# Kernel tuning notes

Measured on AMD Instinct MI355X. Metric: run time of the kernel, lower is better.

Reference implementation:

```python
import jax, jax.numpy as jnp
import numpy as np

GROUP_SIZE = 128


def _dequant_weight(qweight, scales, qzeros, group_size=GROUP_SIZE):
    # qweight: [K//2, N] int, packed nibbles; scales: [K//g, N] fp16; qzeros: [K//2g, N] int
    low = (qweight & 15).astype(jnp.float16)
    high = ((qweight >> 4) & 15).astype(jnp.float16)
    K2, N = qweight.shape
    # interleave even rows = low nibble, odd rows = high nibble -> [K, N]
    w_q = jnp.stack([low, high], axis=1).reshape(2 * K2, N)
    zlow = (qzeros & 15).astype(jnp.float16)
    zhigh = ((qzeros >> 4) & 15).astype(jnp.float16)
    G2, _ = qzeros.shape
    zeros = jnp.stack([zlow, zhigh], axis=1).reshape(2 * G2, N)  # [K//g, N]
    scales_exp = jnp.repeat(scales, group_size, axis=0)          # [K, N]
    zeros_exp = jnp.repeat(zeros, group_size, axis=0)            # [K, N]
    return (w_q - zeros_exp) * scales_exp


def setup_inputs() -> dict:
    key = jax.random.key(0)
    k1, k2, k3, k4 = jax.random.split(key, 4)
    B, S, K, N = 4, 2048, 4096, 11008
    x = jax.random.normal(k1, (B, S, K), dtype=jnp.float16)
    qweight = jax.random.randint(k2, (K // 2, N), 0, 127, dtype=jnp.int32)
    scales = jax.random.uniform(k3, (K // GROUP_SIZE, N), dtype=jnp.float16, minval=0.001, maxval=0.02)
    qzeros = jax.random.randint(k4, (K // GROUP_SIZE // 2, N), 0, 127, dtype=jnp.int32)
    return {"x": x, "qweight": qweight, "scales": scales, "qzeros": qzeros}


def reference(x, qweight, scales, qzeros):
    W = _dequant_weight(qweight, scales, qzeros)  # [K, N] fp16
    return jnp.matmul(x, W)  # [B, S, N]
```

## Files before the change

### kernel.cpp

```cpp
#include <hip/hip_runtime.h>
#include <cstdint>
#include <cstddef>
#include <type_traits>


typedef __bf16 bf16x8 __attribute__((ext_vector_type(8)));
typedef _Float16 halfx8 __attribute__((ext_vector_type(8)));
typedef float floatx4 __attribute__((ext_vector_type(4)));
struct u4 { unsigned x, y, z, w; };

#define M_DIM 8192
#define K_DIM 4096
#define N_DIM 11008
#define BM 128
#define BN 128
#define BK 32

__device__ __forceinline__ unsigned short f2bf(float f) {
  unsigned u = __float_as_uint(f);
  return (unsigned short)((u + 0x7FFFu + ((u >> 16) & 1u)) >> 16);
}
__device__ __forceinline__ float bf2f(unsigned s) { return __uint_as_float(s << 16); }
__device__ __forceinline__ unsigned short f2h(float f) {
  _Float16 h = (_Float16)f;
  return __builtin_bit_cast(unsigned short, h);
}
__device__ __forceinline__ float h2f(unsigned short s) {
  return (float)__builtin_bit_cast(_Float16, s);
}

__global__ void dtype_probe(const unsigned* __restrict__ sd, int* __restrict__ flag) {
  const unsigned lo = sd[threadIdx.x] & 0xFFFFu;
  const int is_bf = (lo >= 0x3A00u) && (lo < 0x3D00u);
  const int is_h  = (lo >= 0x1400u) && (lo < 0x2600u);
  const int f = __all(is_bf) ? 0 : (__all(is_h) ? 2 : 1);
  flag[0] = f;
}

template <int DT>
__launch_bounds__(256, 3)
__global__ void int4gemm_kernel(const void* __restrict__ xv,
                                const int* __restrict__ qw,
                                const void* __restrict__ sv,
                                const int* __restrict__ qz,
                                void* __restrict__ outv,
                                const int* __restrict__ flag) {
  if (*flag != DT) return;

  __shared__ unsigned short As[BM][BK];
  __shared__ unsigned Bs[BN][BK / 2 + 4];
  __shared__ float zoff[32][BN];
  __shared__ float scl[32][BN];

  const int t = threadIdx.x;
  const int m0 = blockIdx.x * BM;
  const int n0 = blockIdx.y * BN;

  for (int i = t; i < 32 * BN; i += 256) {
    const int g = i >> 7, j = i & (BN - 1);
    const int n = n0 + j;
    float s;
    if constexpr (DT == 0)
      s = bf2f(((const unsigned short*)sv)[(size_t)g * N_DIM + n]);
    else if constexpr (DT == 1)
      s = ((const float*)sv)[(size_t)g * N_DIM + n];
    else
      s = h2f(((const unsigned short*)sv)[(size_t)g * N_DIM + n]);
    const int zp = qz[(size_t)(g >> 1) * N_DIM + n];
    const int z = (zp >> ((g & 1) * 4)) & 15;
    zoff[g][j] = 8388608.0f + (float)z;
    scl[g][j] = s;
  }

  const int lane = t & 63;
  const int wid = t >> 6;
  const int wm = (wid >> 1) * 64, wn = (wid & 1) * 64;
  const int lrow = lane & 15, lq = lane >> 4;

  const int mcol = t & 31;
  const int rrow = t >> 5;

  const int c0 = t, c1 = t + 256;

  floatx4 acc[4][4];
#pragma unroll
  for (int mi = 0; mi < 4; ++mi)
#pragma unroll
    for (int ni = 0; ni < 4; ++ni) {
      acc[mi][ni][0] = 0.0f; acc[mi][ni][1] = 0.0f;
      acc[mi][ni][2] = 0.0f; acc[mi][ni][3] = 0.0f;
    }

  __syncthreads();

#pragma unroll 1
  for (int kt = 0; kt < K_DIM / BK; ++kt) {
    const int k0 = kt * BK;

    if constexpr (DT == 1) {
      const float* b0 = (const float*)xv + (size_t)(m0 + (c0 >> 2)) * K_DIM + k0 + ((c0 & 3) << 3);
      const float* b1 = (const float*)xv + (size_t)(m0 + (c1 >> 2)) * K_DIM + k0 + ((c1 & 3) << 3);
      float f0[8], f1[8];
#pragma unroll
      for (int q = 0; q < 8; ++q) f0[q] = b0[q];
#pragma unroll
      for (int q = 0; q < 8; ++q) f1[q] = b1[q];
      u4 p0v, p1v;
      p0v.x = (unsigned)f2bf(f0[0]) | ((unsigned)f2bf(f0[1]) << 16);
      p0v.y = (unsigned)f2bf(f0[2]) | ((unsigned)f2bf(f0[3]) << 16);
      p0v.z = (unsigned)f2bf(f0[4]) | ((unsigned)f2bf(f0[5]) << 16);
      p0v.w = (unsigned)f2bf(f0[6]) | ((unsigned)f2bf(f0[7]) << 16);
      p1v.x = (unsigned)f2bf(f1[0]) | ((unsigned)f2bf(f1[1]) << 16);
      p1v.y = (unsigned)f2bf(f1[2]) | ((unsigned)f2bf(f1[3]) << 16);
      p1v.z = (unsigned)f2bf(f1[4]) | ((unsigned)f2bf(f1[5]) << 16);
      p1v.w = (unsigned)f2bf(f1[6]) | ((unsigned)f2bf(f1[7]) << 16);
      *reinterpret_cast<u4*>(&As[c0 >> 2][(c0 & 3) << 3]) = p0v;
      *reinterpret_cast<u4*>(&As[c1 >> 2][(c1 & 3) << 3]) = p1v;
    } else {
      const unsigned short* xb = (const unsigned short*)xv;
      const u4 a0 = *reinterpret_cast<const u4*>(
          xb + (size_t)(m0 + (c0 >> 2)) * K_DIM + k0 + ((c0 & 3) << 3));
      const u4 a1 = *reinterpret_cast<const u4*>(
          xb + (size_t)(m0 + (c1 >> 2)) * K_DIM + k0 + ((c1 & 3) << 3));
      *reinterpret_cast<u4*>(&As[c0 >> 2][(c0 & 3) << 3]) = a0;
      *reinterpret_cast<u4*>(&As[c1 >> 2][(c1 & 3) << 3]) = a1;
    }

    const int g = k0 >> 7;
    const int* q0 = qw + (size_t)((k0 >> 1) + rrow) * N_DIM + n0 + mcol;
    const int* q1 = q0 + (size_t)8 * N_DIM;
    int p0[4], p1[4];
#pragma unroll
    for (int j = 0; j < 4; ++j) p0[j] = q0[32 * j];
#pragma unroll
    for (int j = 0; j < 4; ++j) p1[j] = q1[32 * j];

#pragma unroll
    for (int j = 0; j < 4; ++j) {
      const int n = mcol + 32 * j;
      const float zo = zoff[g][n], s = scl[g][n];
      const float fl0 = (__uint_as_float((unsigned)(p0[j] & 15) | 0x4B000000u) - zo) * s;
      const float fh0 = (__uint_as_float((unsigned)((p0[j] >> 4) & 15) | 0x4B000000u) - zo) * s;
      const float fl1 = (__uint_as_float((unsigned)(p1[j] & 15) | 0x4B000000u) - zo) * s;
      const float fh1 = (__uint_as_float((unsigned)((p1[j] >> 4) & 15) | 0x4B000000u) - zo) * s;
      unsigned lo0, hi0, lo1, hi1;
      if constexpr (DT == 2) {
        lo0 = f2h(fl0); hi0 = f2h(fh0); lo1 = f2h(fl1); hi1 = f2h(fh1);
      } else {
        lo0 = f2bf(fl0); hi0 = f2bf(fh0); lo1 = f2bf(fl1); hi1 = f2bf(fh1);
      }
      Bs[n][rrow] = lo0 | (hi0 << 16);
      Bs[n][rrow + 8] = lo1 | (hi1 << 16);
    }
    __syncthreads();

    using vecT = typename std::conditional<DT == 2, halfx8, bf16x8>::type;
    vecT av[4], bv[4];
#pragma unroll
    for (int mi = 0; mi < 4; ++mi)
      av[mi] = *reinterpret_cast<const vecT*>(&As[wm + mi * 16 + lrow][lq * 8]);
#pragma unroll
    for (int ni = 0; ni < 4; ++ni)
      bv[ni] = *reinterpret_cast<const vecT*>(&Bs[wn + ni * 16 + lrow][lq * 4]);
#pragma unroll
    for (int mi = 0; mi < 4; ++mi)
#pragma unroll
      for (int ni = 0; ni < 4; ++ni) {
        if constexpr (DT == 2)
          acc[mi][ni] = __builtin_amdgcn_mfma_f32_16x16x32_f16(av[mi], bv[ni],
                                                               acc[mi][ni], 0, 0, 0);
        else
          acc[mi][ni] = __builtin_amdgcn_mfma_f32_16x16x32_bf16(av[mi], bv[ni],
                                                                acc[mi][ni], 0, 0, 0);
      }
    __syncthreads();
  }

#pragma unroll
  for (int mi = 0; mi < 4; ++mi) {
#pragma unroll
    for (int rr = 0; rr < 4; ++rr) {
      const size_t rowoff = (size_t)(m0 + wm + mi * 16 + lq * 4 + rr) * N_DIM;
#pragma unroll
      for (int ni = 0; ni < 4; ++ni) {
        const size_t idx = rowoff + n0 + wn + ni * 16 + lrow;
        const float v = acc[mi][ni][rr];
        if constexpr (DT == 0)
          ((unsigned short*)outv)[idx] = f2bf(v);
        else if constexpr (DT == 1)
          ((float*)outv)[idx] = v;
        else
          ((unsigned short*)outv)[idx] = f2h(v);
      }
    }
  }
}

extern "C" void kernel_launch(void* const* d_in, const int* in_sizes, int n_in,
                              void* d_out, int out_size, void* d_ws, size_t ws_size,
                              hipStream_t stream) {
  const void* x = d_in[0];
  const int* qw = (const int*)d_in[1];
  const void* sc = d_in[2];
  const int* qz = (const int*)d_in[3];
  int* flag = (int*)d_ws;

  dtype_probe<<<1, 64, 0, stream>>>((const unsigned*)sc, flag);

  dim3 grid(M_DIM / BM, N_DIM / BN);
  int4gemm_kernel<0><<<grid, dim3(256), 0, stream>>>(x, qw, sc, qz, d_out, flag);
  int4gemm_kernel<1><<<grid, dim3(256), 0, stream>>>(x, qw, sc, qz, d_out, flag);
  int4gemm_kernel<2><<<grid, dim3(256), 0, stream>>>(x, qw, sc, qz, d_out, flag);
}
```

Before: 1.808 ms.

## Load A tile via global_load_lds with swizzle, packed fp16 dequant, occupancy 4

Activations are now copied straight from global memory into LDS with global_load_lds, using an XOR swizzle on the column slot to avoid bank conflicts. The read side uses the matching swizzled offset. The fp16 path dequantizes two nibbles at once with packed half math, using the 0x6400 magic-number trick and a combined scale/zero table, and the bf16 paths use the hardware v_cvt_pk_bf16_f32 instruction. Launch bounds are raised to 4 waves per SIMD and the shared-memory tables are shrunk so that occupancy can fit. The tradeoffs are tighter register pressure and fp16 rounding in the dequant subtraction.

Result: faster. 1.738 ms (-3.8%).

```diff
diff --git a/kernel.cpp b/kernel.cpp
--- a/kernel.cpp
+++ b/kernel.cpp
@@ -6,6 +6,7 @@
 
 typedef __bf16 bf16x8 __attribute__((ext_vector_type(8)));
 typedef _Float16 halfx8 __attribute__((ext_vector_type(8)));
+typedef _Float16 h2 __attribute__((ext_vector_type(2)));
 typedef float floatx4 __attribute__((ext_vector_type(4)));
 struct u4 { unsigned x, y, z, w; };
 
@@ -28,6 +29,11 @@
 __device__ __forceinline__ float h2f(unsigned short s) {
   return (float)__builtin_bit_cast(_Float16, s);
 }
+__device__ __forceinline__ unsigned cvt_pk_bf16(float lo, float hi) {
+  unsigned r;
+  asm("v_cvt_pk_bf16_f32 %0, %1, %2" : "=v"(r) : "v"(lo), "v"(hi));
+  return r;
+}
 
 __global__ void dtype_probe(const unsigned* __restrict__ sd, int* __restrict__ flag) {
   const unsigned lo = sd[threadIdx.x] & 0xFFFFu;
@@ -38,7 +44,7 @@
 }
 
 template <int DT>
-__launch_bounds__(256, 3)
+__launch_bounds__(256, 4)
 __global__ void int4gemm_kernel(const void* __restrict__ xv,
                                 const int* __restrict__ qw,
                                 const void* __restrict__ sv,
@@ -47,10 +53,9 @@
                                 const int* __restrict__ flag) {
   if (*flag != DT) return;
 
-  __shared__ unsigned short As[BM][BK];
-  __shared__ unsigned Bs[BN][BK / 2 + 4];
-  __shared__ float zoff[32][BN];
-  __shared__ float scl[32][BN];
+  __shared__ __align__(16) unsigned short As[BM * BK];
+  __shared__ __align__(16) unsigned Bs[BN][BK / 2 + 4];
+  __shared__ unsigned tbl[(DT == 2) ? (32 * BN) : (64 * BN)];
 
   const int t = threadIdx.x;
   const int m0 = blockIdx.x * BM;
@@ -59,28 +64,38 @@
   for (int i = t; i < 32 * BN; i += 256) {
     const int g = i >> 7, j = i & (BN - 1);
     const int n = n0 + j;
-    float s;
-    if constexpr (DT == 0)
-      s = bf2f(((const unsigned short*)sv)[(size_t)g * N_DIM + n]);
-    else if constexpr (DT == 1)
-      s = ((const float*)sv)[(size_t)g * N_DIM + n];
-    else
-      s = h2f(((const unsigned short*)sv)[(size_t)g * N_DIM + n]);
     const int zp = qz[(size_t)(g >> 1) * N_DIM + n];
     const int z = (zp >> ((g & 1) * 4)) & 15;
-    zoff[g][j] = 8388608.0f + (float)z;
-    scl[g][j] = s;
+    if constexpr (DT == 2) {
+      const unsigned sb = ((const unsigned short*)sv)[(size_t)g * N_DIM + n];
+      tbl[i] = sb | ((unsigned)f2h(1024.0f + (float)z) << 16);
+    } else {
+      float s;
+      if constexpr (DT == 0)
+        s = bf2f(((const unsigned short*)sv)[(size_t)g * N_DIM + n]);
+      else
+        s = ((const float*)sv)[(size_t)g * N_DIM + n];
+      tbl[i] = __float_as_uint(8388608.0f + (float)z);
+      tbl[32 * BN + i] = __float_as_uint(s);
+    }
   }
 
   const int lane = t & 63;
   const int wid = t >> 6;
   const int wm = (wid >> 1) * 64, wn = (wid & 1) * 64;
   const int lrow = lane & 15, lq = lane >> 4;
+  const int aslot = ((lq ^ ((lrow >> 1) & 3)) << 3);
 
   const int mcol = t & 31;
   const int rrow = t >> 5;
 
-  const int c0 = t, c1 = t + 256;
+  const int arow = t >> 2;
+  const int acol = (((t & 3) ^ ((arow >> 1) & 3)) << 3);
+  const unsigned short* xb = (const unsigned short*)xv;
+  const unsigned short* ga0 = xb + (size_t)(m0 + arow) * K_DIM + acol;
+  const unsigned short* ga1 = ga0 + (size_t)64 * K_DIM;
+  char* lA0 = (char*)As + (wid << 10);
+  char* lA1 = lA0 + 4096;
 
   floatx4 acc[4][4];
 #pragma unroll
@@ -96,35 +111,6 @@
 #pragma unroll 1
   for (int kt = 0; kt < K_DIM / BK; ++kt) {
     const int k0 = kt * BK;
-
-    if constexpr (DT == 1) {
-      const float* b0 = (const float*)xv + (size_t)(m0 + (c0 >> 2)) * K_DIM + k0 + ((c0 & 3) << 3);
-      const float* b1 = (const float*)xv + (size_t)(m0 + (c1 >> 2)) * K_DIM + k0 + ((c1 & 3) << 3);
-      float f0[8], f1[8];
-#pragma unroll
-      for (int q = 0; q < 8; ++q) f0[q] = b0[q];
-#pragma unroll
-      for (int q = 0; q < 8; ++q) f1[q] = b1[q];
-      u4 p0v, p1v;
-      p0v.x = (unsigned)f2bf(f0[0]) | ((unsigned)f2bf(f0[1]) << 16);
-      p0v.y = (unsigned)f2bf(f0[2]) | ((unsigned)f2bf(f0[3]) << 16);
-      p0v.z = (unsigned)f2bf(f0[4]) | ((unsigned)f2bf(f0[5]) << 16);
-      p0v.w = (unsigned)f2bf(f0[6]) | ((unsigned)f2bf(f0[7]) << 16);
-      p1v.x = (unsigned)f2bf(f1[0]) | ((unsigned)f2bf(f1[1]) << 16);
-      p1v.y = (unsigned)f2bf(f1[2]) | ((unsigned)f2bf(f1[3]) << 16);
-      p1v.z = (unsigned)f2bf(f1[4]) | ((unsigned)f2bf(f1[5]) << 16);
-      p1v.w = (unsigned)f2bf(f1[6]) | ((unsigned)f2bf(f1[7]) << 16);
-      *reinterpret_cast<u4*>(&As[c0 >> 2][(c0 & 3) << 3]) = p0v;
-      *reinterpret_cast<u4*>(&As[c1 >> 2][(c1 & 3) << 3]) = p1v;
-    } else {
-      const unsigned short* xb = (const unsigned short*)xv;
-      const u4 a0 = *reinterpret_cast<const u4*>(
-          xb + (size_t)(m0 + (c0 >> 2)) * K_DIM + k0 + ((c0 & 3) << 3));
-      const u4 a1 = *reinterpret_cast<const u4*>(
-          xb + (size_t)(m0 + (c1 >> 2)) * K_DIM + k0 + ((c1 & 3) << 3));
-      *reinterpret_cast<u4*>(&As[c0 >> 2][(c0 & 3) << 3]) = a0;
-      *reinterpret_cast<u4*>(&As[c1 >> 2][(c1 & 3) << 3]) = a1;
-    }
 
     const int g = k0 >> 7;
     const int* q0 = qw + (size_t)((k0 >> 1) + rrow) * N_DIM + n0 + mcol;
@@ -135,22 +121,55 @@
 #pragma unroll
     for (int j = 0; j < 4; ++j) p1[j] = q1[32 * j];
 
+    if constexpr (DT != 1) {
+      __builtin_amdgcn_global_load_lds(
+          (const __attribute__((address_space(1))) unsigned*)(ga0 + k0),
+          (__attribute__((address_space(3))) unsigned*)lA0, 16, 0, 0);
+      __builtin_amdgcn_global_load_lds(
+          (const __attribute__((address_space(1))) unsigned*)(ga1 + k0),
+          (__attribute__((address_space(3))) unsigned*)lA1, 16, 0, 0);
+    } else {
+      const float* xf = (const float*)xv;
+      const float* gf0 = xf + (size_t)(m0 + arow) * K_DIM + k0 + acol;
+      const float* gf1 = gf0 + (size_t)64 * K_DIM;
+      floatx4 fa = *(const floatx4*)gf0, fb = *(const floatx4*)(gf0 + 4);
+      floatx4 fc = *(const floatx4*)gf1, fd = *(const floatx4*)(gf1 + 4);
+      u4 p0v, p1v;
+      p0v.x = cvt_pk_bf16(fa[0], fa[1]); p0v.y = cvt_pk_bf16(fa[2], fa[3]);
+      p0v.z = cvt_pk_bf16(fb[0], fb[1]); p0v.w = cvt_pk_bf16(fb[2], fb[3]);
+      p1v.x = cvt_pk_bf16(fc[0], fc[1]); p1v.y = cvt_pk_bf16(fc[2], fc[3]);
+      p1v.z = cvt_pk_bf16(fd[0], fd[1]); p1v.w = cvt_pk_bf16(fd[2], fd[3]);
+      *reinterpret_cast<u4*>((char*)As + t * 16) = p0v;
+      *reinterpret_cast<u4*>((char*)As + t * 16 + 4096) = p1v;
+    }
+
 #pragma unroll
     for (int j = 0; j < 4; ++j) {
       const int n = mcol + 32 * j;
-      const float zo = zoff[g][n], s = scl[g][n];
-      const float fl0 = (__uint_as_float((unsigned)(p0[j] & 15) | 0x4B000000u) - zo) * s;
-      const float fh0 = (__uint_as_float((unsigned)((p0[j] >> 4) & 15) | 0x4B000000u) - zo) * s;
-      const float fl1 = (__uint_as_float((unsigned)(p1[j] & 15) | 0x4B000000u) - zo) * s;
-      const float fh1 = (__uint_as_float((unsigned)((p1[j] >> 4) & 15) | 0x4B000000u) - zo) * s;
-      unsigned lo0, hi0, lo1, hi1;
       if constexpr (DT == 2) {
-        lo0 = f2h(fl0); hi0 = f2h(fh0); lo1 = f2h(fl1); hi1 = f2h(fh1);
+        const unsigned ts = tbl[(g << 7) + n];
+        const unsigned s2 = __builtin_amdgcn_perm(ts, ts, 0x01000100u);
+        const unsigned z2 = __builtin_amdgcn_perm(ts, ts, 0x03020302u);
+        const h2 zh = __builtin_bit_cast(h2, z2);
+        const h2 sh = __builtin_bit_cast(h2, s2);
+        const unsigned P0 = (unsigned)p0[j], P1 = (unsigned)p1[j];
+        const unsigned q20 = ((P0 & 15u) | ((P0 << 12) & 0xF0000u)) | 0x64006400u;
+        const unsigned q21 = ((P1 & 15u) | ((P1 << 12) & 0xF0000u)) | 0x64006400u;
+        const h2 w0 = (__builtin_bit_cast(h2, q20) - zh) * sh;
+        const h2 w1 = (__builtin_bit_cast(h2, q21) - zh) * sh;
+        Bs[n][rrow] = __builtin_bit_cast(unsigned, w0);
+        Bs[n][rrow + 8] = __builtin_bit_cast(unsigned, w1);
       } else {
-        lo0 = f2bf(fl0); hi0 = f2bf(fh0); lo1 = f2bf(fl1); hi1 = f2bf(fh1);
+        const float zo = __uint_as_float(tbl[(g << 7) + n]);
+        const float s = __uint_as_float(tbl[32 * BN + (g << 7) + n]);
+        const unsigned P0 = (unsigned)p0[j], P1 = (unsigned)p1[j];
+        const float fl0 = (__uint_as_float((P0 & 15u) | 0x4B000000u) - zo) * s;
+        const float fh0 = (__uint_as_float(((P0 >> 4) & 15u) | 0x4B000000u) - zo) * s;
+        const float fl1 = (__uint_as_float((P1 & 15u) | 0x4B000000u) - zo) * s;
+        const float fh1 = (__uint_as_float(((P1 >> 4) & 15u) | 0x4B000000u) - zo) * s;
+        Bs[n][rrow] = cvt_pk_bf16(fl0, fh0);
+        Bs[n][rrow + 8] = cvt_pk_bf16(fl1, fh1);
       }
-      Bs[n][rrow] = lo0 | (hi0 << 16);
-      Bs[n][rrow + 8] = lo1 | (hi1 << 16);
     }
     __syncthreads();
 
@@ -158,7 +177,7 @@
     vecT av[4], bv[4];
 #pragma unroll
     for (int mi = 0; mi < 4; ++mi)
-      av[mi] = *reinterpret_cast<const vecT*>(&As[wm + mi * 16 + lrow][lq * 8]);
+      av[mi] = *reinterpret_cast<const vecT*>(&As[(wm + mi * 16 + lrow) * BK + aslot]);
 #pragma unroll
     for (int ni = 0; ni < 4; ++ni)
       bv[ni] = *reinterpret_cast<const vecT*>(&Bs[wn + ni * 16 + lrow][lq * 4]);
```
